# Kernel tuning notes

Hardware: AMD Instinct MI355X
Metric: run time of the kernel (lower is better)

## Reference

```python
import jax, jax.numpy as jnp
import numpy as np

B, C, H, W = 1, 512, 24, 24
N_HEADS, WS = 8, 7
PAD = WS // 2
HEAD_DIM = C // N_HEADS


def setup_inputs() -> dict:
    key = jax.random.key(0)
    ks = jax.random.split(key, 7)
    s = 0.02
    return {
        "x": jax.random.normal(ks[0], (B, C, H, W), dtype=jnp.float32),
        "Wq": s * jax.random.normal(ks[1], (C, C), dtype=jnp.float32),
        "bq": s * jax.random.normal(ks[2], (C,), dtype=jnp.float32),
        "Wk": s * jax.random.normal(ks[3], (C, C), dtype=jnp.float32),
        "bk": s * jax.random.normal(ks[4], (C,), dtype=jnp.float32),
        "Wv": s * jax.random.normal(ks[5], (C, C), dtype=jnp.float32),
        "bv": s * jax.random.normal(ks[6], (C,), dtype=jnp.float32),
        # module initializes gamma to zero; use small nonzero so output depends on attention
        "gamma": jnp.full((1,), 0.1, dtype=jnp.float32),
    }


def _conv1x1(z, Wt, bt):
    # 1x1 Conv2d == per-pixel GEMM over channels
    return jnp.einsum("bchw,oc->bohw", z, Wt) + bt[None, :, None, None]


def _windows(z):
    # z: (B, C, H+ws-1, W+ws-1) -> (B, n_heads, head_dim, ws*ws*H*W)
    # matches torch unfold(2,ws,1).unfold(3,ws,1).permute(0,1,4,5,2,3).view(...)
    taps = [z[:, :, di:di + H, dj:dj + W] for di in range(WS) for dj in range(WS)]
    w = jnp.stack(taps, axis=2)  # (B, C, ws*ws, H, W)
    return w.reshape(B, N_HEADS, HEAD_DIM, WS * WS * H * W)


def reference(x, Wq, bq, Wk, bk, Wv, bv, gamma):
    q = _conv1x1(x, Wq, bq).reshape(B, N_HEADS, HEAD_DIM, H * W)  # (B,h,d,HW)
    xp = jnp.pad(x, ((0, 0), (0, 0), (PAD, PAD), (PAD, PAD)), mode="reflect")
    k = _windows(_conv1x1(xp, Wk, bk))  # (B,h,d,ws^2*HW)
    v = _windows(_conv1x1(xp, Wv, bv))  # (B,h,d,ws^2*HW)
    # NOTE: as written in the source, each query attends to ALL ws^2*H*W keys
    energy = jnp.einsum("bhdq,bhdk->bhqk", q, k)  # (B,h,HW,ws^2*HW)
    attn = jax.nn.softmax(energy, axis=-1)
    out_w = jnp.einsum("bhqk,bhdk->bhdq", attn, v).reshape(B, C, H, W)
    return gamma * out_w + x
```

## Files before the change

kernel.cpp:

```cpp
#include <hip/hip_runtime.h>

#define HW   576
#define CC   512
#define PW   30
#define PPK  1024

typedef float f32x4 __attribute__((ext_vector_type(4)));
typedef short s16x8 __attribute__((ext_vector_type(8)));

__device__ __forceinline__ unsigned short f2bf(float f) {
    unsigned u = __float_as_uint(f);
    return (unsigned short)((u + 0x7FFFu + ((u >> 16) & 1u)) >> 16);
}
__device__ __forceinline__ float bf2f(unsigned short h) {
    return __uint_as_float((unsigned)h << 16);
}
__device__ __forceinline__ int smapf(int p) {
    if (p >= 900) return 576;
    const int y = p / PW, xw = p - y * PW;
    int iy = y - 3;  iy = (iy < 0) ? -iy : (iy > 23 ? 46 - iy : iy);
    int ix = xw - 3; ix = (ix < 0) ? -ix : (ix > 23 ? 46 - ix : ix);
    return iy * 24 + ix;
}

#define OFF_QT 0u
#define OFF_KT 589824u
#define OFF_VP 1638400u
#define OFF_XT 2686976u
#define OFF_WB 3277824u

__global__ __launch_bounds__(256) void cvtT(
    const float* __restrict__ x,
    const float* __restrict__ Wq, const float* __restrict__ Wk,
    const float* __restrict__ Wv,
    unsigned short* __restrict__ xT, unsigned short* __restrict__ wb)
{
    const int b = blockIdx.x, t = threadIdx.x;
    if (b < 72) {
        __shared__ float tile[64][65];
        const int pt = b % 9, ct = b / 9;
        const int p0 = pt * 64, c0 = ct * 64;
        const int tr = t >> 4, tc4 = (t & 15) * 4;
        #pragma unroll
        for (int cr = 0; cr < 4; ++cr) {
            const int row = cr * 16 + tr;
            const float4 v = *(const float4*)&x[(size_t)(c0 + row) * HW + p0 + tc4];
            tile[row][tc4 + 0] = v.x;
            tile[row][tc4 + 1] = v.y;
            tile[row][tc4 + 2] = v.z;
            tile[row][tc4 + 3] = v.w;
        }
        __syncthreads();
        #pragma unroll
        for (int cr = 0; cr < 4; ++cr) {
            const int prow = cr * 16 + tr;
            ushort4 o;
            o.x = f2bf(tile[tc4 + 0][prow]);
            o.y = f2bf(tile[tc4 + 1][prow]);
            o.z = f2bf(tile[tc4 + 2][prow]);
            o.w = f2bf(tile[tc4 + 3][prow]);
            *(ushort4*)&xT[(size_t)(p0 + prow) * CC + c0 + tc4] = o;
        }
    } else if (b == 72) {
        if (t < 128) *(ushort4*)&xT[(size_t)576 * CC + t * 4] = (ushort4){0, 0, 0, 0};
    } else {
        const int wi = (b - 73) * 2048 + t * 8;
        const int sel = wi >> 18, off = wi & 262143;
        const float* src = (sel == 0) ? Wq : (sel == 1) ? Wk : Wv;
        const float4 v0 = *(const float4*)&src[off];
        const float4 v1 = *(const float4*)&src[off + 4];
        ushort4 o0, o1;
        o0.x = f2bf(v0.x); o0.y = f2bf(v0.y); o0.z = f2bf(v0.z); o0.w = f2bf(v0.w);
        o1.x = f2bf(v1.x); o1.y = f2bf(v1.y); o1.z = f2bf(v1.z); o1.w = f2bf(v1.w);
        *(ushort4*)&wb[wi]     = o0;
        *(ushort4*)&wb[wi + 4] = o1;
    }
}

__global__ __launch_bounds__(256) void qkv_ks(
    const unsigned short* __restrict__ xT, const unsigned short* __restrict__ wb,
    const float* __restrict__ bq, const float* __restrict__ bk,
    const float* __restrict__ bv,
    unsigned short* __restrict__ qT, unsigned short* __restrict__ kT,
    unsigned short* __restrict__ vP)
{
    const int b = blockIdx.x;
    const int t = threadIdx.x;
    const int lane = t & 63, w = t >> 6;
    const int fr = lane & 15, u = lane >> 4;

    int sel, m0, n0;
    if (b < 288)      { sel = 0; m0 = (b >> 4) << 5;               n0 = (b & 15) << 5; }
    else if (b < 800) { const int k = b - 288; sel = 1; m0 = (k >> 4) << 5; n0 = (k & 15) << 5; }
    else              { const int k = b - 800; sel = 2; m0 = (k >> 5) << 5; n0 = (k & 31) << 5; }

    const unsigned short *A, *B;
    int ar0, ar1, bn0, bn1;
    if (sel == 0)      { A = xT;          B = wb;
                         ar0 = m0 + fr;         ar1 = m0 + 16 + fr;
                         bn0 = n0 + fr;         bn1 = n0 + 16 + fr; }
    else if (sel == 1) { A = xT;          B = wb + 262144;
                         ar0 = smapf(m0 + fr);  ar1 = smapf(m0 + 16 + fr);
                         bn0 = n0 + fr;         bn1 = n0 + 16 + fr; }
    else               { A = wb + 524288; B = xT;
                         ar0 = m0 + fr;         ar1 = m0 + 16 + fr;
                         bn0 = smapf(n0 + fr);  bn1 = smapf(n0 + 16 + fr); }

    const int kw = w * 128;
    const unsigned short* Ap0 = A + (size_t)ar0 * CC + kw + u * 8;
    const unsigned short* Ap1 = A + (size_t)ar1 * CC + kw + u * 8;
    const unsigned short* Bp0 = B + (size_t)bn0 * CC + kw + u * 8;
    const unsigned short* Bp1 = B + (size_t)bn1 * CC + kw + u * 8;

    f32x4 acc00 = (f32x4){0.f, 0.f, 0.f, 0.f};
    f32x4 acc01 = (f32x4){0.f, 0.f, 0.f, 0.f};
    f32x4 acc10 = (f32x4){0.f, 0.f, 0.f, 0.f};
    f32x4 acc11 = (f32x4){0.f, 0.f, 0.f, 0.f};
    #pragma unroll
    for (int k0 = 0; k0 < 128; k0 += 32) {
        const s16x8 a0 = *(const s16x8*)(Ap0 + k0);
        const s16x8 a1 = *(const s16x8*)(Ap1 + k0);
        const s16x8 b0 = *(const s16x8*)(Bp0 + k0);
        const s16x8 b1 = *(const s16x8*)(Bp1 + k0);
        acc00 = __builtin_amdgcn_mfma_f32_16x16x32_bf16(a0, b0, acc00, 0, 0, 0);
        acc01 = __builtin_amdgcn_mfma_f32_16x16x32_bf16(a0, b1, acc01, 0, 0, 0);
        acc10 = __builtin_amdgcn_mfma_f32_16x16x32_bf16(a1, b0, acc10, 0, 0, 0);
        acc11 = __builtin_amdgcn_mfma_f32_16x16x32_bf16(a1, b1, acc11, 0, 0, 0);
    }

    __shared__ __align__(16) f32x4 red[4][4][64];
    red[w][0][lane] = acc00;
    red[w][1][lane] = acc01;
    red[w][2][lane] = acc10;
    red[w][3][lane] = acc11;
    __syncthreads();

    f32x4 v = red[0][w][lane];
    #pragma unroll
    for (int w2 = 1; w2 < 4; ++w2) v = v + red[w2][w][lane];

    const int mi = w >> 1, ni = w & 1;
    const int n = n0 + ni * 16 + fr;
    #pragma unroll
    for (int r = 0; r < 4; ++r) {
        const int m = m0 + mi * 16 + u * 4 + r;
        if (sel == 0) {
            qT[((size_t)(n >> 6) * HW + m) * 64 + (n & 63)] = f2bf(v[r] + bq[n]);
        } else if (sel == 1) {
            kT[((size_t)(n >> 6) * PPK + m) * 64 + (n & 63)] = f2bf(v[r] + bk[n]);
        } else {
            vP[((size_t)(m >> 6) * 64 + (m & 63)) * PPK + n] = f2bf(v[r] + bv[m]);
        }
    }
}

#define WLS 1040
__global__ __launch_bounds__(512) void attn7(
    const unsigned short* __restrict__ qT, const unsigned short* __restrict__ kT,
    const unsigned short* __restrict__ vP, const float* __restrict__ x,
    const float* __restrict__ gamma, float* __restrict__ out)
{
    const int q0 = blockIdx.x * 16;
    const int hd = blockIdx.y;
    const int t  = threadIdx.x;
    const int lane = t & 63, w = t >> 6;
    const int fr = lane & 15, u = lane >> 4;

    __shared__ float cnt_s[PPK];
    __shared__ __align__(16) unsigned short Wl[16 * WLS];
    __shared__ float lw[128], sca[16];
    __shared__ float4 red[4][64];

    #pragma unroll
    for (int j = 0; j < 2; ++j) {
        const int i = w * 128 + j * 64 + lane;
        float c = 0.f;
        if (i < 900) {
            const int y = i / PW, xw = i - y * PW;
            int cy = y + 1;  if (PW - y  < cy) cy = PW - y;  if (cy > 7) cy = 7;
            int cx = xw + 1; if (PW - xw < cx) cx = PW - xw; if (cx > 7) cx = 7;
            c = (float)(cy * cx);
        }
        cnt_s[i] = c;
    }

    const unsigned short* qrow = qT + ((size_t)hd * HW + q0 + fr) * 64 + u * 8;
    const s16x8 b0 = *(const s16x8*)qrow;
    const s16x8 b1 = *(const s16x8*)(qrow + 32);

    f32x4 e[8];
    #pragma unroll
    for (int t4 = 0; t4 < 8; ++t4) {
        const unsigned short* krow =
            kT + ((size_t)hd * PPK + w * 128 + t4 * 16 + fr) * 64 + u * 8;
        const s16x8 a0 = *(const s16x8*)krow;
        const s16x8 a1 = *(const s16x8*)(krow + 32);
        f32x4 a = (f32x4){0.f, 0.f, 0.f, 0.f};
        a = __builtin_amdgcn_mfma_f32_16x16x32_bf16(a0, b0, a, 0, 0, 0);
        a = __builtin_amdgcn_mfma_f32_16x16x32_bf16(a1, b1, a, 0, 0, 0);
        e[t4] = a;
    }

    float sum = 0.f;
    #pragma unroll
    for (int t4 = 0; t4 < 8; ++t4) {
        const float4 c4 = *(const float4*)&cnt_s[w * 128 + t4 * 16 + u * 4];
        const float cw[4] = {c4.x, c4.y, c4.z, c4.w};
        unsigned short wb4[4];
        #pragma unroll
        for (int r = 0; r < 4; ++r) {
            const float wv2 = cw[r] * __expf(e[t4][r]);
            sum += wv2;
            wb4[r] = f2bf(wv2);
        }
        const int ho = fr * WLS + w * 128 + t4 * 16 + u * 4;
        *(unsigned*)&Wl[ho]     = (unsigned)wb4[0] | ((unsigned)wb4[1] << 16);
        *(unsigned*)&Wl[ho + 2] = (unsigned)wb4[2] | ((unsigned)wb4[3] << 16);
    }
    sum += __shfl_xor(sum, 16);
    sum += __shfl_xor(sum, 32);
    if (lane < 16) lw[w * 16 + lane] = sum;
    __syncthreads();

    if (t < 16) {
        float lq = 0.f;
        #pragma unroll
        for (int j = 0; j < 8; ++j) lq += lw[j * 16 + t];
        sca[t] = gamma[0] / lq;
    }

    const int dt = w & 3, ph = w >> 2;
    f32x4 oA = (f32x4){0.f, 0.f, 0.f, 0.f};
    f32x4 oB = (f32x4){0.f, 0.f, 0.f, 0.f};
    const unsigned short* vrow =
        vP + ((size_t)hd * 64 + dt * 16 + fr) * PPK + ph * 512 + u * 8;
    const unsigned short* wrow = &Wl[fr * WLS + ph * 512 + u * 8];
    #pragma unroll
    for (int c = 0; c < 8; ++c) {
        const s16x8 awA = *(const s16x8*)(wrow + c * 64);
        const s16x8 bvA = *(const s16x8*)(vrow + c * 64);
        const s16x8 awB = *(const s16x8*)(wrow + c * 64 + 32);
        const s16x8 bvB = *(const s16x8*)(vrow + c * 64 + 32);
        oA = __builtin_amdgcn_mfma_f32_16x16x32_bf16(awA, bvA, oA, 0, 0, 0);
        oB = __builtin_amdgcn_mfma_f32_16x16x32_bf16(awB, bvB, oB, 0, 0, 0);
    }
    const f32x4 o = oA + oB;
    if (w >= 4) red[dt][lane] = (float4){o[0], o[1], o[2], o[3]};
    __syncthreads();
    if (w >= 4) return;

    const float4 r2 = red[dt][lane];
    const int d = hd * 64 + dt * 16 + fr;
    const size_t gb = (size_t)d * HW + q0 + u * 4;
    const float4 x4 = *(const float4*)&x[gb];
    float4 o4;
    o4.x = fmaf(sca[u * 4 + 0], o[0] + r2.x, x4.x);
    o4.y = fmaf(sca[u * 4 + 1], o[1] + r2.y, x4.y);
    o4.z = fmaf(sca[u * 4 + 2], o[2] + r2.z, x4.z);
    o4.w = fmaf(sca[u * 4 + 3], o[3] + r2.w, x4.w);
    *(float4*)&out[gb] = o4;
}

extern "C" void kernel_launch(void* const* d_in, const int* in_sizes, int n_in,
                              void* d_out, int out_size, void* d_ws, size_t ws_size,
                              hipStream_t stream) {
    const float* x     = (const float*)d_in[0];
    const float* Wq    = (const float*)d_in[1];
    const float* bq    = (const float*)d_in[2];
    const float* Wk    = (const float*)d_in[3];
    const float* bk    = (const float*)d_in[4];
    const float* Wv    = (const float*)d_in[5];
    const float* bv    = (const float*)d_in[6];
    const float* gamma = (const float*)d_in[7];
    float* out = (float*)d_out;

    char* wsb = (char*)d_ws;
    unsigned short* qT = (unsigned short*)(wsb + OFF_QT);
    unsigned short* kT = (unsigned short*)(wsb + OFF_KT);
    unsigned short* vP = (unsigned short*)(wsb + OFF_VP);
    unsigned short* xT = (unsigned short*)(wsb + OFF_XT);
    unsigned short* wb = (unsigned short*)(wsb + OFF_WB);

    cvtT<<<dim3(457), 256, 0, stream>>>(x, Wq, Wk, Wv, xT, wb);
    qkv_ks<<<dim3(1312), 256, 0, stream>>>(xT, wb, bq, bk, bv, qT, kT, vP);
    attn7<<<dim3(36, 8), 512, 0, stream>>>(qT, kT, vP, x, gamma, out);
}
```

Baseline: 103.0 us.

## Collapse padded key positions into per-source-pixel multiplicities for K/V

Every padded (reflect) key position maps to some original pixel. The change therefore computes K and V only for the 576 source pixels and weights each one by its total multiplicity across all windows and reflections, a separable product of per-axis counts. Before, it used 1024 padded positions (900 real) weighted by window coverage counts. This cuts the K/V projection GEMM blocks and the attention key length from 1024 to 576. The cost is uneven work across waves (5 vs 4 tiles) and a more intricate multiplicity formula that must be exact.

```diff
diff --git a/kernel.cpp b/kernel.cpp
--- a/kernel.cpp
+++ b/kernel.cpp
@@ -2,8 +2,7 @@
 
 #define HW   576
 #define CC   512
-#define PW   30
-#define PPK  1024
+#define NP   576
 
 typedef float f32x4 __attribute__((ext_vector_type(4)));
 typedef short s16x8 __attribute__((ext_vector_type(8)));
@@ -15,19 +14,18 @@
 __device__ __forceinline__ float bf2f(unsigned short h) {
     return __uint_as_float((unsigned)h << 16);
 }
-__device__ __forceinline__ int smapf(int p) {
-    if (p >= 900) return 576;
-    const int y = p / PW, xw = p - y * PW;
-    int iy = y - 3;  iy = (iy < 0) ? -iy : (iy > 23 ? 46 - iy : iy);
-    int ix = xw - 3; ix = (ix < 0) ? -ix : (ix > 23 ? 46 - ix : ix);
-    return iy * 24 + ix;
+__device__ __forceinline__ float maxis(int s) {
+    int c = s + 4; if (27 - s < c) c = 27 - s; if (c > 7) c = 7;
+    if (s >= 1 && s <= 3)  c += 4 - s;
+    if (s >= 20 && s <= 22) c += s - 19;
+    return (float)c;
 }
 
 #define OFF_QT 0u
 #define OFF_KT 589824u
-#define OFF_VP 1638400u
-#define OFF_XT 2686976u
-#define OFF_WB 3277824u
+#define OFF_VP 1179648u
+#define OFF_XT 1769472u
+#define OFF_WB 2359296u
 
 __global__ __launch_bounds__(256) void cvtT(
     const float* __restrict__ x,
@@ -61,10 +59,8 @@
             o.w = f2bf(tile[tc4 + 3][prow]);
             *(ushort4*)&xT[(size_t)(p0 + prow) * CC + c0 + tc4] = o;
         }
-    } else if (b == 72) {
-        if (t < 128) *(ushort4*)&xT[(size_t)576 * CC + t * 4] = (ushort4){0, 0, 0, 0};
     } else {
-        const int wi = (b - 73) * 2048 + t * 8;
+        const int wi = (b - 72) * 2048 + t * 8;
         const int sel = wi >> 18, off = wi & 262143;
         const float* src = (sel == 0) ? Wq : (sel == 1) ? Wk : Wv;
         const float4 v0 = *(const float4*)&src[off];
@@ -91,26 +87,19 @@
 
     int sel, m0, n0;
     if (b < 288)      { sel = 0; m0 = (b >> 4) << 5;               n0 = (b & 15) << 5; }
-    else if (b < 800) { const int k = b - 288; sel = 1; m0 = (k >> 4) << 5; n0 = (k & 15) << 5; }
-    else              { const int k = b - 800; sel = 2; m0 = (k >> 5) << 5; n0 = (k & 31) << 5; }
+    else if (b < 576) { const int k = b - 288; sel = 1; m0 = (k >> 4) << 5; n0 = (k & 15) << 5; }
+    else              { const int k = b - 576; sel = 2; m0 = (k & 15) << 5; n0 = (k >> 4) << 5; }
 
     const unsigned short *A, *B;
-    int ar0, ar1, bn0, bn1;
-    if (sel == 0)      { A = xT;          B = wb;
-                         ar0 = m0 + fr;         ar1 = m0 + 16 + fr;
-                         bn0 = n0 + fr;         bn1 = n0 + 16 + fr; }
-    else if (sel == 1) { A = xT;          B = wb + 262144;
-                         ar0 = smapf(m0 + fr);  ar1 = smapf(m0 + 16 + fr);
-                         bn0 = n0 + fr;         bn1 = n0 + 16 + fr; }
-    else               { A = wb + 524288; B = xT;
-                         ar0 = m0 + fr;         ar1 = m0 + 16 + fr;
-                         bn0 = smapf(n0 + fr);  bn1 = smapf(n0 + 16 + fr); }
+    if (sel == 0)      { A = xT;          B = wb; }
+    else if (sel == 1) { A = xT;          B = wb + 262144; }
+    else               { A = wb + 524288; B = xT; }
 
     const int kw = w * 128;
-    const unsigned short* Ap0 = A + (size_t)ar0 * CC + kw + u * 8;
-    const unsigned short* Ap1 = A + (size_t)ar1 * CC + kw + u * 8;
-    const unsigned short* Bp0 = B + (size_t)bn0 * CC + kw + u * 8;
-    const unsigned short* Bp1 = B + (size_t)bn1 * CC + kw + u * 8;
+    const unsigned short* Ap0 = A + (size_t)(m0 + fr)      * CC + kw + u * 8;
+    const unsigned short* Ap1 = A + (size_t)(m0 + 16 + fr) * CC + kw + u * 8;
+    const unsigned short* Bp0 = B + (size_t)(n0 + fr)      * CC + kw + u * 8;
+    const unsigned short* Bp1 = B + (size_t)(n0 + 16 + fr) * CC + kw + u * 8;
 
     f32x4 acc00 = (f32x4){0.f, 0.f, 0.f, 0.f};
     f32x4 acc01 = (f32x4){0.f, 0.f, 0.f, 0.f};
@@ -147,15 +136,15 @@
         if (sel == 0) {
             qT[((size_t)(n >> 6) * HW + m) * 64 + (n & 63)] = f2bf(v[r] + bq[n]);
         } else if (sel == 1) {
-            kT[((size_t)(n >> 6) * PPK + m) * 64 + (n & 63)] = f2bf(v[r] + bk[n]);
+            kT[((size_t)(n >> 6) * NP + m) * 64 + (n & 63)] = f2bf(v[r] + bk[n]);
         } else {
-            vP[((size_t)(m >> 6) * 64 + (m & 63)) * PPK + n] = f2bf(v[r] + bv[m]);
-        }
-    }
-}
-
-#define WLS 1040
-__global__ __launch_bounds__(512) void attn7(
+            vP[((size_t)(m >> 6) * 64 + (m & 63)) * NP + n] = f2bf(v[r] + bv[m]);
+        }
+    }
+}
+
+#define WLS 592
+__global__ __launch_bounds__(512) void attn8(
     const unsigned short* __restrict__ qT, const unsigned short* __restrict__ kT,
     const unsigned short* __restrict__ vP, const float* __restrict__ x,
     const float* __restrict__ gamma, float* __restrict__ out)
@@ -166,56 +155,61 @@
     const int lane = t & 63, w = t >> 6;
     const int fr = lane & 15, u = lane >> 4;
 
-    __shared__ float cnt_s[PPK];
+    __shared__ float mult_s[NP];
     __shared__ __align__(16) unsigned short Wl[16 * WLS];
     __shared__ float lw[128], sca[16];
     __shared__ float4 red[4][64];
 
+    const int ntw = (w < 4) ? 5 : 4;
+    const int off = (w < 4) ? w * 80 : 320 + (w - 4) * 64;
+    const int sz  = ntw * 16;
+
     #pragma unroll
     for (int j = 0; j < 2; ++j) {
-        const int i = w * 128 + j * 64 + lane;
-        float c = 0.f;
-        if (i < 900) {
-            const int y = i / PW, xw = i - y * PW;
-            int cy = y + 1;  if (PW - y  < cy) cy = PW - y;  if (cy > 7) cy = 7;
-            int cx = xw + 1; if (PW - xw < cx) cx = PW - xw; if (cx > 7) cx = 7;
-            c = (float)(cy * cx);
-        }
-        cnt_s[i] = c;
+        const int li = j * 64 + lane;
+        if (li < sz) {
+            const int i = off + li;
+            const int sy = i / 24, sx = i - sy * 24;
+            mult_s[i] = maxis(sy) * maxis(sx);
+        }
     }
 
     const unsigned short* qrow = qT + ((size_t)hd * HW + q0 + fr) * 64 + u * 8;
     const s16x8 b0 = *(const s16x8*)qrow;
     const s16x8 b1 = *(const s16x8*)(qrow + 32);
 
-    f32x4 e[8];
-    #pragma unroll
-    for (int t4 = 0; t4 < 8; ++t4) {
-        const unsigned short* krow =
-            kT + ((size_t)hd * PPK + w * 128 + t4 * 16 + fr) * 64 + u * 8;
-        const s16x8 a0 = *(const s16x8*)krow;
-        const s16x8 a1 = *(const s16x8*)(krow + 32);
-        f32x4 a = (f32x4){0.f, 0.f, 0.f, 0.f};
-        a = __builtin_amdgcn_mfma_f32_16x16x32_bf16(a0, b0, a, 0, 0, 0);
-        a = __builtin_amdgcn_mfma_f32_16x16x32_bf16(a1, b1, a, 0, 0, 0);
-        e[t4] = a;
+    f32x4 e[5];
+    #pragma unroll
+    for (int t4 = 0; t4 < 5; ++t4) {
+        if (t4 < ntw) {
+            const unsigned short* krow =
+                kT + ((size_t)hd * NP + off + t4 * 16 + fr) * 64 + u * 8;
+            const s16x8 a0 = *(const s16x8*)krow;
+            const s16x8 a1 = *(const s16x8*)(krow + 32);
+            f32x4 a = (f32x4){0.f, 0.f, 0.f, 0.f};
+            a = __builtin_amdgcn_mfma_f32_16x16x32_bf16(a0, b0, a, 0, 0, 0);
+            a = __builtin_amdgcn_mfma_f32_16x16x32_bf16(a1, b1, a, 0, 0, 0);
+            e[t4] = a;
+        }
     }
 
     float sum = 0.f;
     #pragma unroll
-    for (int t4 = 0; t4 < 8; ++t4) {
-        const float4 c4 = *(const float4*)&cnt_s[w * 128 + t4 * 16 + u * 4];
-        const float cw[4] = {c4.x, c4.y, c4.z, c4.w};
-        unsigned short wb4[4];
-        #pragma unroll
-        for (int r = 0; r < 4; ++r) {
-            const float wv2 = cw[r] * __expf(e[t4][r]);
-            sum += wv2;
-            wb4[r] = f2bf(wv2);
-        }
-        const int ho = fr * WLS + w * 128 + t4 * 16 + u * 4;
-        *(unsigned*)&Wl[ho]     = (unsigned)wb4[0] | ((unsigned)wb4[1] << 16);
-        *(unsigned*)&Wl[ho + 2] = (unsigned)wb4[2] | ((unsigned)wb4[3] << 16);
+    for (int t4 = 0; t4 < 5; ++t4) {
+        if (t4 < ntw) {
+            const float4 c4 = *(const float4*)&mult_s[off + t4 * 16 + u * 4];
+            const float cw[4] = {c4.x, c4.y, c4.z, c4.w};
+            unsigned short wb4[4];
+            #pragma unroll
+            for (int r = 0; r < 4; ++r) {
+                const float wv2 = cw[r] * __expf(e[t4][r]);
+                sum += wv2;
+                wb4[r] = f2bf(wv2);
+            }
+            const int ho = fr * WLS + off + t4 * 16 + u * 4;
+            *(unsigned*)&Wl[ho]     = (unsigned)wb4[0] | ((unsigned)wb4[1] << 16);
+            *(unsigned*)&Wl[ho + 2] = (unsigned)wb4[2] | ((unsigned)wb4[3] << 16);
+        }
     }
     sum += __shfl_xor(sum, 16);
     sum += __shfl_xor(sum, 32);
@@ -230,19 +224,18 @@
     }
 
     const int dt = w & 3, ph = w >> 2;
+    const int poff = ph * 288;
     f32x4 oA = (f32x4){0.f, 0.f, 0.f, 0.f};
     f32x4 oB = (f32x4){0.f, 0.f, 0.f, 0.f};
     const unsigned short* vrow =
-        vP + ((size_t)hd * 64 + dt * 16 + fr) * PPK + ph * 512 + u * 8;
-    const unsigned short* wrow = &Wl[fr * WLS + ph * 512 + u * 8];
-    #pragma unroll
-    for (int c = 0; c < 8; ++c) {
-        const s16x8 awA = *(const s16x8*)(wrow + c * 64);
-        const s16x8 bvA = *(const s16x8*)(vrow + c * 64);
-        const s16x8 awB = *(const s16x8*)(wrow + c * 64 + 32);
-        const s16x8 bvB = *(const s16x8*)(vrow + c * 64 + 32);
-        oA = __builtin_amdgcn_mfma_f32_16x16x32_bf16(awA, bvA, oA, 0, 0, 0);
-        oB = __builtin_amdgcn_mfma_f32_16x16x32_bf16(awB, bvB, oB, 0, 0, 0);
+        vP + ((size_t)hd * 64 + dt * 16 + fr) * NP + poff + u * 8;
+    const unsigned short* wrow = &Wl[fr * WLS + poff + u * 8];
+    #pragma unroll
+    for (int c = 0; c < 9; ++c) {
+        const s16x8 aw = *(const s16x8*)(wrow + c * 32);
+        const s16x8 bv2 = *(const s16x8*)(vrow + c * 32);
+        if (c & 1) oB = __builtin_amdgcn_mfma_f32_16x16x32_bf16(aw, bv2, oB, 0, 0, 0);
+        else       oA = __builtin_amdgcn_mfma_f32_16x16x32_bf16(aw, bv2, oA, 0, 0, 0);
     }
     const f32x4 o = oA + oB;
     if (w >= 4) red[dt][lane] = (float4){o[0], o[1], o[2], o[3]};
@@ -281,7 +274,7 @@
     unsigned short* xT = (unsigned short*)(wsb + OFF_XT);
     unsigned short* wb = (unsigned short*)(wsb + OFF_WB);
 
-    cvtT<<<dim3(457), 256, 0, stream>>>(x, Wq, Wk, Wv, xT, wb);
-    qkv_ks<<<dim3(1312), 256, 0, stream>>>(xT, wb, bq, bk, bv, qT, kT, vP);
-    attn7<<<dim3(36, 8), 512, 0, stream>>>(qT, kT, vP, x, gamma, out);
-}
+    cvtT<<<dim3(456), 256, 0, stream>>>(x, Wq, Wk, Wv, xT, wb);
+    qkv_ks<<<dim3(864), 256, 0, stream>>>(xT, wb, bq, bk, bv, qT, kT, vP);
+    attn8<<<dim3(36, 8), 512, 0, stream>>>(qT, kT, vP, x, gamma, out);
+}
```

Measured after the change: 91.58 us (median of 2 runs). 11.1% less time.
